# Kernel optimization log

Hardware: AMD Instinct MI355X
Metric: run time of the kernel (lower is better)

The kernel has to match this reference:

```python
import jax, jax.numpy as jnp
import numpy as np

D_MODEL = 1024
NUM_HEADS = 16
D_K = D_MODEL // NUM_HEADS


def setup_inputs() -> dict:
    key = jax.random.key(0)
    ks = jax.random.split(key, 5)
    B, S = 4, 2048
    scale = 1.0 / np.sqrt(D_MODEL)
    x = jax.random.normal(ks[0], (B, S, D_MODEL), dtype=jnp.float32)
    # Linear(d_model, d_model, bias=False) weights, stored as [out, in] like torch
    Wq = jax.random.normal(ks[1], (D_MODEL, D_MODEL), dtype=jnp.float32) * scale
    Wk = jax.random.normal(ks[2], (D_MODEL, D_MODEL), dtype=jnp.float32) * scale
    Wv = jax.random.normal(ks[3], (D_MODEL, D_MODEL), dtype=jnp.float32) * scale
    Wo = jax.random.normal(ks[4], (D_MODEL, D_MODEL), dtype=jnp.float32) * scale
    return {"x": x, "Wq": Wq, "Wk": Wk, "Wv": Wv, "Wo": Wo}


def reference(x, Wq, Wk, Wv, Wo):
    B, S, D = x.shape
    H, dk = NUM_HEADS, D_K
    # projections (torch Linear: x @ W.T)
    q = (x @ Wq.T).reshape(B, S, H, dk).transpose(0, 2, 1, 3)  # [B,H,S,dk]
    k = (x @ Wk.T).reshape(B, S, H, dk).transpose(0, 2, 1, 3)
    v = (x @ Wv.T).reshape(B, S, H, dk).transpose(0, 2, 1, 3)
    scores = jnp.einsum("bhqd,bhkd->bhqk", q, k) / jnp.sqrt(jnp.float32(dk))
    causal = jnp.triu(jnp.ones((S, S), dtype=bool), k=1)  # True above diagonal -> masked
    scores = jnp.where(causal[None, None], -jnp.inf, scores)
    attn = jax.nn.softmax(scores, axis=-1)
    out = jnp.einsum("bhqk,bhkd->bhqd", attn, v)  # [B,H,S,dk]
    out = out.transpose(0, 2, 1, 3).reshape(B, S, D)
    return out @ Wo.T
```

## Files before the change

kernel.cpp:

```cpp
#include <hip/hip_runtime.h>

typedef __bf16 bf16_t;
typedef __bf16 bf16x8 __attribute__((ext_vector_type(8)));
typedef __bf16 bf16x4 __attribute__((ext_vector_type(4)));
typedef float f32x4 __attribute__((ext_vector_type(4)));
typedef unsigned short u16x8 __attribute__((ext_vector_type(8)));

#define AS1C(p) ((const __attribute__((address_space(1))) void*)(p))
#define AS3(p) ((__attribute__((address_space(3))) void*)(p))

__device__ __forceinline__ unsigned short f2b_rne(float f) {
  union { float f; unsigned u; } x; x.f = f;
  unsigned u = x.u;
  u += 0x7fffu + ((u >> 16) & 1u);
  return (unsigned short)(u >> 16);
}

__device__ __forceinline__ float fast_exp2(float x) {
  return __builtin_amdgcn_exp2f(x);
}

__global__ __launch_bounds__(256) void cast_f32_bf16(const float* __restrict__ in,
                                                     unsigned short* __restrict__ out,
                                                     int n) {
  int i = (blockIdx.x * 256 + threadIdx.x) * 8;
  if (i >= n) return;
  const float4* p = reinterpret_cast<const float4*>(in + i);
  float4 a = p[0], b = p[1];
  u16x8 o;
  o[0] = f2b_rne(a.x); o[1] = f2b_rne(a.y); o[2] = f2b_rne(a.z); o[3] = f2b_rne(a.w);
  o[4] = f2b_rne(b.x); o[5] = f2b_rne(b.y); o[6] = f2b_rne(b.z); o[7] = f2b_rne(b.w);
  *reinterpret_cast<u16x8*>(out + i) = o;
}

__global__ __launch_bounds__(256) void cast_w4(const float* __restrict__ w0,
                                               const float* __restrict__ w1,
                                               const float* __restrict__ w2,
                                               const float* __restrict__ w3,
                                               unsigned short* __restrict__ out) {
  const float* in = (blockIdx.y == 0) ? w0 : (blockIdx.y == 1) ? w1
                  : (blockIdx.y == 2) ? w2 : w3;
  int i = (blockIdx.x * 256 + threadIdx.x) * 8;
  unsigned short* o = out + (size_t)blockIdx.y * (1024u * 1024u);
  const float4* p = reinterpret_cast<const float4*>(in + i);
  float4 a = p[0], b = p[1];
  u16x8 v;
  v[0] = f2b_rne(a.x); v[1] = f2b_rne(a.y); v[2] = f2b_rne(a.z); v[3] = f2b_rne(a.w);
  v[4] = f2b_rne(b.x); v[5] = f2b_rne(b.y); v[6] = f2b_rne(b.z); v[7] = f2b_rne(b.w);
  *reinterpret_cast<u16x8*>(o + i) = v;
}

template <int OUT_F32>
__global__ __launch_bounds__(256) void gemm_bt(const bf16_t* __restrict__ A,
                                               const bf16_t* __restrict__ Bm,
                                               void* __restrict__ C,
                                               int M, int N, int K, int lda,
                                               float scale, int qlim) {
  __shared__ bf16_t As[128 * 32];
  __shared__ bf16_t Bs[128 * 32];
  const int tid = threadIdx.x;
  const int lane = tid & 63, wave = tid >> 6;
  const int wm = wave >> 1, wn = wave & 1;
  const int r = lane & 15, kg = lane >> 4;
  const int m0 = blockIdx.y * 128, n0 = blockIdx.x * 128;
  const float sc = (n0 < qlim) ? scale : 1.0f;
  f32x4 acc[4][4] = {};
  const size_t abase = (size_t)m0 * lda;
  const size_t bbase = (size_t)n0 * K;
  for (int k0 = 0; k0 < K; k0 += 32) {
#pragma unroll
    for (int c = 0; c < 2; ++c) {
      int e = (c * 256 + tid) * 8;
      int rr = e >> 5, cc = e & 31;
      __builtin_amdgcn_global_load_lds(AS1C(A + abase + (size_t)rr * lda + k0 + cc),
                                       AS3(As + (c * 256 + wave * 64) * 8), 16, 0, 0);
      __builtin_amdgcn_global_load_lds(AS1C(Bm + bbase + (size_t)rr * K + k0 + cc),
                                       AS3(Bs + (c * 256 + wave * 64) * 8), 16, 0, 0);
    }
    __syncthreads();
    bf16x8 af[4], bfr[4];
#pragma unroll
    for (int t = 0; t < 4; ++t) {
      af[t]  = *reinterpret_cast<const bf16x8*>(As + (wm * 64 + t * 16 + r) * 32 + kg * 8);
      bfr[t] = *reinterpret_cast<const bf16x8*>(Bs + (wn * 64 + t * 16 + r) * 32 + kg * 8);
    }
    __builtin_amdgcn_s_setprio(1);
#pragma unroll
    for (int i = 0; i < 4; ++i)
#pragma unroll
      for (int j = 0; j < 4; ++j)
        acc[i][j] = __builtin_amdgcn_mfma_f32_16x16x32_bf16(af[i], bfr[j], acc[i][j], 0, 0, 0);
    __builtin_amdgcn_s_setprio(0);
    __syncthreads();
  }
#pragma unroll
  for (int i = 0; i < 4; ++i) {
#pragma unroll
    for (int j = 0; j < 4; ++j) {
      const int mb = m0 + wm * 64 + i * 16 + kg * 4;
      const int nc = n0 + wn * 64 + j * 16 + r;
#pragma unroll
      for (int v = 0; v < 4; ++v) {
        float val = acc[i][j][v] * sc;
        size_t idx = (size_t)(mb + v) * N + nc;
        if (OUT_F32) reinterpret_cast<float*>(C)[idx] = val;
        else reinterpret_cast<unsigned short*>(C)[idx] = f2b_rne(val);
      }
    }
  }
}

__global__ __launch_bounds__(256) void transpose_v(const bf16_t* __restrict__ qkv,
                                                   bf16_t* __restrict__ vt) {
  __shared__ bf16_t Vs[64 * 72];
  const int t = threadIdx.x;
  const int s0 = blockIdx.x * 64;
  const int bh = blockIdx.y;
  const int b = bh >> 4, h = bh & 15;
  const size_t in_base = ((size_t)b * 2048 + s0) * 3072 + 2048 + h * 64;
#pragma unroll
  for (int c = 0; c < 2; ++c) {
    int chunk = c * 256 + t;
    int ss = chunk >> 3, dd = (chunk & 7) * 8;
    bf16x8 v = *reinterpret_cast<const bf16x8*>(qkv + in_base + (size_t)ss * 3072 + dd);
    *reinterpret_cast<bf16x8*>(Vs + ss * 72 + dd) = v;
  }
  __syncthreads();
  const size_t out_base = (size_t)bh * 64 * 2048 + s0;
#pragma unroll
  for (int c = 0; c < 2; ++c) {
    int chunk = c * 256 + t;
    int dd = chunk >> 3, ss = (chunk & 7) * 8;
    bf16x8 o;
#pragma unroll
    for (int j = 0; j < 8; ++j) o[j] = Vs[(ss + j) * 72 + dd];
    *reinterpret_cast<bf16x8*>(vt + out_base + (size_t)dd * 2048 + ss) = o;
  }
}

__global__ __launch_bounds__(512) void flash_attn(const bf16_t* __restrict__ QKV,
                                                  const bf16_t* __restrict__ VT,
                                                  unsigned short* __restrict__ O,
                                                  int ostride) {
  __shared__ bf16_t Ks[64 * 72];
  __shared__ bf16_t Vts[64 * 72];
  __shared__ bf16_t Pl[8][16 * 72];
  const int tid = threadIdx.x;
  const int lane = tid & 63, wave = tid >> 6;
  const int r = lane & 15, kg = lane >> 4;
  const int xcd = blockIdx.x & 7;
  const int bh = xcd * 8 + (blockIdx.y & 7);
  const int qt = 15 - ((blockIdx.x >> 3) * 8 + (blockIdx.y >> 3));
  const int b = bh >> 4, h = bh & 15;
  const size_t qkv_row0 = (size_t)b * 2048 * 3072;
  const int qcol = h * 64, kcol = 1024 + h * 64;
  const size_t vt_base = (size_t)bh * 64 * 2048;
  const size_t o_row0 = (size_t)b * 2048 * ostride;
  const int ocol = h * 64;
  const int srr = tid >> 3, scc = (tid & 7) * 8;

  const int q0 = qt * 128;
  const int qrow = q0 + wave * 16 + r;
  const int tmax_w = (q0 + wave * 16 + 15) >> 6;
  const int ntiles = qt * 2 + 2;

  const size_t qoff = qkv_row0 + (size_t)qrow * 3072 + qcol;
  bf16x8 qf0 = *reinterpret_cast<const bf16x8*>(QKV + qoff + kg * 8);
  bf16x8 qf1 = *reinterpret_cast<const bf16x8*>(QKV + qoff + 32 + kg * 8);

  f32x4 oacc[4] = {};
  float m_run = -3e30f, l_run = 0.f;

  bf16x8 gk = *reinterpret_cast<const bf16x8*>(QKV + qkv_row0 + (size_t)srr * 3072 + kcol + scc);
  bf16x8 gv = *reinterpret_cast<const bf16x8*>(VT + vt_base + (size_t)srr * 2048 + scc);

  for (int t = 0; t < ntiles; ++t) {
    __syncthreads();
    *reinterpret_cast<bf16x8*>(Ks + srr * 72 + scc) = gk;
    *reinterpret_cast<bf16x8*>(Vts + srr * 72 + scc) = gv;
    __syncthreads();
    if (t + 1 < ntiles) {
      const int kv1 = (t + 1) * 64;
      gk = *reinterpret_cast<const bf16x8*>(QKV + qkv_row0 + (size_t)(kv1 + srr) * 3072 + kcol + scc);
      gv = *reinterpret_cast<const bf16x8*>(VT + vt_base + (size_t)srr * 2048 + kv1 + scc);
    }
    if (t > tmax_w) continue;

    const int kv0 = t * 64;
    float vals[16];
#pragma unroll
    for (int nt = 0; nt < 4; ++nt) {
      bf16x8 kf0 = *reinterpret_cast<const bf16x8*>(Ks + (nt * 16 + r) * 72 + kg * 8);
      bf16x8 kf1 = *reinterpret_cast<const bf16x8*>(Ks + (nt * 16 + r) * 72 + 32 + kg * 8);
      f32x4 s = {};
      __builtin_amdgcn_s_setprio(1);
      s = __builtin_amdgcn_mfma_f32_16x16x32_bf16(kf0, qf0, s, 0, 0, 0);
      s = __builtin_amdgcn_mfma_f32_16x16x32_bf16(kf1, qf1, s, 0, 0, 0);
      __builtin_amdgcn_s_setprio(0);
#pragma unroll
      for (int v = 0; v < 4; ++v) vals[nt * 4 + v] = s[v];
    }
    if (t == tmax_w) {
#pragma unroll
      for (int nt = 0; nt < 4; ++nt)
#pragma unroll
        for (int v = 0; v < 4; ++v)
          if (kv0 + nt * 16 + kg * 4 + v > qrow) vals[nt * 4 + v] = -3e30f;
    }
    float a0 = fmaxf(fmaxf(vals[0], vals[1]), vals[2]);
    float a1 = fmaxf(fmaxf(vals[3], vals[4]), vals[5]);
    float a2 = fmaxf(fmaxf(vals[6], vals[7]), vals[8]);
    float a3 = fmaxf(fmaxf(vals[9], vals[10]), vals[11]);
    float a4 = fmaxf(fmaxf(vals[12], vals[13]), vals[14]);
    float pmax = fmaxf(fmaxf(fmaxf(a0, a1), fmaxf(a2, a3)), fmaxf(a4, vals[15]));
    pmax = fmaxf(pmax, __shfl_xor(pmax, 16));
    pmax = fmaxf(pmax, __shfl_xor(pmax, 32));
    if (!__all(pmax <= m_run + 8.0f)) {
      const float m_new = fmaxf(m_run, pmax);
      const float alpha = fast_exp2(m_run - m_new);
      l_run *= alpha;
      f32x4 al;
#pragma unroll
      for (int v = 0; v < 4; ++v) al[v] = __shfl(alpha, kg * 4 + v);
#pragma unroll
      for (int dt = 0; dt < 4; ++dt)
#pragma unroll
        for (int v = 0; v < 4; ++v) oacc[dt][v] *= al[v];
      m_run = m_new;
    }
    float psum = 0.f;
#pragma unroll
    for (int ii = 0; ii < 16; ++ii) {
      float p = fast_exp2(vals[ii] - m_run);
      vals[ii] = p;
      psum += p;
    }
    psum += __shfl_xor(psum, 16);
    psum += __shfl_xor(psum, 32);
    l_run += psum;

#pragma unroll
    for (int nt = 0; nt < 4; ++nt) {
      bf16x4 pb;
#pragma unroll
      for (int v = 0; v < 4; ++v) pb[v] = (bf16_t)vals[nt * 4 + v];
      *reinterpret_cast<bf16x4*>(&Pl[wave][r * 72 + nt * 16 + kg * 4]) = pb;
    }
    bf16x8 pa0 = *reinterpret_cast<const bf16x8*>(&Pl[wave][r * 72 + kg * 8]);
    bf16x8 pa1 = *reinterpret_cast<const bf16x8*>(&Pl[wave][r * 72 + 32 + kg * 8]);

#pragma unroll
    for (int dt = 0; dt < 4; ++dt) {
      bf16x8 vb0 = *reinterpret_cast<const bf16x8*>(Vts + (dt * 16 + r) * 72 + kg * 8);
      bf16x8 vb1 = *reinterpret_cast<const bf16x8*>(Vts + (dt * 16 + r) * 72 + 32 + kg * 8);
      __builtin_amdgcn_s_setprio(1);
      oacc[dt] = __builtin_amdgcn_mfma_f32_16x16x32_bf16(pa0, vb0, oacc[dt], 0, 0, 0);
      oacc[dt] = __builtin_amdgcn_mfma_f32_16x16x32_bf16(pa1, vb1, oacc[dt], 0, 0, 0);
      __builtin_amdgcn_s_setprio(0);
    }
  }

  const float linv = 1.0f / l_run;
  f32x4 il;
#pragma unroll
  for (int v = 0; v < 4; ++v) il[v] = __shfl(linv, kg * 4 + v);
  const size_t orow0 = o_row0 + (size_t)(q0 + wave * 16) * ostride + ocol;
#pragma unroll
  for (int dt = 0; dt < 4; ++dt) {
    const int d = dt * 16 + r;
#pragma unroll
    for (int v = 0; v < 4; ++v)
      O[orow0 + (size_t)(kg * 4 + v) * ostride + d] = f2b_rne(oacc[dt][v] * il[v]);
  }
}

extern "C" void kernel_launch(void* const* d_in, const int* in_sizes, int n_in,
                              void* d_out, int out_size, void* d_ws, size_t ws_size,
                              hipStream_t stream) {
  const float* x  = (const float*)d_in[0];
  const float* Wq = (const float*)d_in[1];
  const float* Wk = (const float*)d_in[2];
  const float* Wv = (const float*)d_in[3];
  const float* Wo = (const float*)d_in[4];

  char* ws = (char*)d_ws;
  bf16_t* xb  = (bf16_t*)(ws);
  bf16_t* wqb = (bf16_t*)(ws + (16u << 20));
  bf16_t* wob = (bf16_t*)(ws + (22u << 20));
  bf16_t* qkv = (bf16_t*)(ws + (24u << 20));
  bf16_t* vt  = (bf16_t*)(ws);

  const int NX = 4 * 2048 * 1024;
  cast_f32_bf16<<<NX / 2048, 256, 0, stream>>>(x, (unsigned short*)xb, NX);
  cast_w4<<<dim3(512, 4), 256, 0, stream>>>(Wq, Wk, Wv, Wo, (unsigned short*)wqb);

  gemm_bt<0><<<dim3(3072 / 128, 8192 / 128), 256, 0, stream>>>(
      xb, wqb, qkv, 8192, 3072, 1024, 1024, 0.18033688011112042f, 1024);

  transpose_v<<<dim3(2048 / 64, 64), 256, 0, stream>>>(qkv, vt);

  flash_attn<<<dim3(16, 64), 512, 0, stream>>>(qkv, vt, (unsigned short*)qkv, 3072);

  gemm_bt<1><<<dim3(1024 / 128, 8192 / 128), 256, 0, stream>>>(
      qkv, wob, d_out, 8192, 1024, 1024, 3072, 1.0f, 0);
}
```

Baseline: 213.9 us.

## Pair causal query tiles per block and double-buffer K/V tiles in LDS

Each flash-attention block now handles two query tiles, qt and 15-qt, one after the other. This balances the causal workload across blocks, with a 64x8 grid instead of 16x64, and drops the previous XCD-aware block remapping. K and V shared-memory tiles are double-buffered so each iteration needs one barrier instead of two. The row-sum reduction is deferred to the end as a per-lane partial sum, and the max shuffles run only when a rescale is needed. The risks are fewer blocks in flight, lost L2 locality from the old XCD mapping, and more LDS use per block.

```diff
diff --git a/kernel.cpp b/kernel.cpp
--- a/kernel.cpp
+++ b/kernel.cpp
@@ -142,15 +142,14 @@
                                                   const bf16_t* __restrict__ VT,
                                                   unsigned short* __restrict__ O,
                                                   int ostride) {
-  __shared__ bf16_t Ks[64 * 72];
-  __shared__ bf16_t Vts[64 * 72];
+  __shared__ bf16_t Ks[2][64 * 72];
+  __shared__ bf16_t Vts[2][64 * 72];
   __shared__ bf16_t Pl[8][16 * 72];
   const int tid = threadIdx.x;
   const int lane = tid & 63, wave = tid >> 6;
   const int r = lane & 15, kg = lane >> 4;
-  const int xcd = blockIdx.x & 7;
-  const int bh = xcd * 8 + (blockIdx.y & 7);
-  const int qt = 15 - ((blockIdx.x >> 3) * 8 + (blockIdx.y >> 3));
+  const int bh = blockIdx.x;
+  const int pair = blockIdx.y;
   const int b = bh >> 4, h = bh & 15;
   const size_t qkv_row0 = (size_t)b * 2048 * 3072;
   const int qcol = h * 64, kcol = 1024 + h * 64;
@@ -159,118 +158,120 @@
   const int ocol = h * 64;
   const int srr = tid >> 3, scc = (tid & 7) * 8;
 
-  const int q0 = qt * 128;
-  const int qrow = q0 + wave * 16 + r;
-  const int tmax_w = (q0 + wave * 16 + 15) >> 6;
-  const int ntiles = qt * 2 + 2;
-
-  const size_t qoff = qkv_row0 + (size_t)qrow * 3072 + qcol;
-  bf16x8 qf0 = *reinterpret_cast<const bf16x8*>(QKV + qoff + kg * 8);
-  bf16x8 qf1 = *reinterpret_cast<const bf16x8*>(QKV + qoff + 32 + kg * 8);
-
-  f32x4 oacc[4] = {};
-  float m_run = -3e30f, l_run = 0.f;
-
-  bf16x8 gk = *reinterpret_cast<const bf16x8*>(QKV + qkv_row0 + (size_t)srr * 3072 + kcol + scc);
-  bf16x8 gv = *reinterpret_cast<const bf16x8*>(VT + vt_base + (size_t)srr * 2048 + scc);
-
-  for (int t = 0; t < ntiles; ++t) {
-    __syncthreads();
-    *reinterpret_cast<bf16x8*>(Ks + srr * 72 + scc) = gk;
-    *reinterpret_cast<bf16x8*>(Vts + srr * 72 + scc) = gv;
-    __syncthreads();
-    if (t + 1 < ntiles) {
-      const int kv1 = (t + 1) * 64;
-      gk = *reinterpret_cast<const bf16x8*>(QKV + qkv_row0 + (size_t)(kv1 + srr) * 3072 + kcol + scc);
-      gv = *reinterpret_cast<const bf16x8*>(VT + vt_base + (size_t)srr * 2048 + kv1 + scc);
-    }
-    if (t > tmax_w) continue;
-
-    const int kv0 = t * 64;
-    float vals[16];
-#pragma unroll
-    for (int nt = 0; nt < 4; ++nt) {
-      bf16x8 kf0 = *reinterpret_cast<const bf16x8*>(Ks + (nt * 16 + r) * 72 + kg * 8);
-      bf16x8 kf1 = *reinterpret_cast<const bf16x8*>(Ks + (nt * 16 + r) * 72 + 32 + kg * 8);
-      f32x4 s = {};
-      __builtin_amdgcn_s_setprio(1);
-      s = __builtin_amdgcn_mfma_f32_16x16x32_bf16(kf0, qf0, s, 0, 0, 0);
-      s = __builtin_amdgcn_mfma_f32_16x16x32_bf16(kf1, qf1, s, 0, 0, 0);
-      __builtin_amdgcn_s_setprio(0);
-#pragma unroll
-      for (int v = 0; v < 4; ++v) vals[nt * 4 + v] = s[v];
-    }
-    if (t == tmax_w) {
-#pragma unroll
-      for (int nt = 0; nt < 4; ++nt)
-#pragma unroll
-        for (int v = 0; v < 4; ++v)
-          if (kv0 + nt * 16 + kg * 4 + v > qrow) vals[nt * 4 + v] = -3e30f;
-    }
-    float a0 = fmaxf(fmaxf(vals[0], vals[1]), vals[2]);
-    float a1 = fmaxf(fmaxf(vals[3], vals[4]), vals[5]);
-    float a2 = fmaxf(fmaxf(vals[6], vals[7]), vals[8]);
-    float a3 = fmaxf(fmaxf(vals[9], vals[10]), vals[11]);
-    float a4 = fmaxf(fmaxf(vals[12], vals[13]), vals[14]);
-    float pmax = fmaxf(fmaxf(fmaxf(a0, a1), fmaxf(a2, a3)), fmaxf(a4, vals[15]));
-    pmax = fmaxf(pmax, __shfl_xor(pmax, 16));
-    pmax = fmaxf(pmax, __shfl_xor(pmax, 32));
-    if (!__all(pmax <= m_run + 8.0f)) {
-      const float m_new = fmaxf(m_run, pmax);
-      const float alpha = fast_exp2(m_run - m_new);
-      l_run *= alpha;
-      f32x4 al;
-#pragma unroll
-      for (int v = 0; v < 4; ++v) al[v] = __shfl(alpha, kg * 4 + v);
-#pragma unroll
-      for (int dt = 0; dt < 4; ++dt)
-#pragma unroll
-        for (int v = 0; v < 4; ++v) oacc[dt][v] *= al[v];
-      m_run = m_new;
-    }
-    float psum = 0.f;
-#pragma unroll
-    for (int ii = 0; ii < 16; ++ii) {
-      float p = fast_exp2(vals[ii] - m_run);
-      vals[ii] = p;
-      psum += p;
-    }
-    psum += __shfl_xor(psum, 16);
-    psum += __shfl_xor(psum, 32);
-    l_run += psum;
-
-#pragma unroll
-    for (int nt = 0; nt < 4; ++nt) {
-      bf16x4 pb;
-#pragma unroll
-      for (int v = 0; v < 4; ++v) pb[v] = (bf16_t)vals[nt * 4 + v];
-      *reinterpret_cast<bf16x4*>(&Pl[wave][r * 72 + nt * 16 + kg * 4]) = pb;
-    }
-    bf16x8 pa0 = *reinterpret_cast<const bf16x8*>(&Pl[wave][r * 72 + kg * 8]);
-    bf16x8 pa1 = *reinterpret_cast<const bf16x8*>(&Pl[wave][r * 72 + 32 + kg * 8]);
-
+  for (int pass = 0; pass < 2; ++pass) {
+    const int qt = pass ? (15 - pair) : pair;
+    const int q0 = qt * 128;
+    const int qrow = q0 + wave * 16 + r;
+    const int tmax_w = (q0 + wave * 16 + 15) >> 6;
+    const int ntiles = qt * 2 + 2;
+
+    const size_t qoff = qkv_row0 + (size_t)qrow * 3072 + qcol;
+    bf16x8 qf0 = *reinterpret_cast<const bf16x8*>(QKV + qoff + kg * 8);
+    bf16x8 qf1 = *reinterpret_cast<const bf16x8*>(QKV + qoff + 32 + kg * 8);
+
+    f32x4 oacc[4] = {};
+    float m_run = -3e30f, l_lane = 0.f;
+
+    bf16x8 gk = *reinterpret_cast<const bf16x8*>(QKV + qkv_row0 + (size_t)srr * 3072 + kcol + scc);
+    bf16x8 gv = *reinterpret_cast<const bf16x8*>(VT + vt_base + (size_t)srr * 2048 + scc);
+
+    for (int t = 0; t < ntiles; ++t) {
+      const int buf = t & 1;
+      *reinterpret_cast<bf16x8*>(&Ks[buf][srr * 72 + scc]) = gk;
+      *reinterpret_cast<bf16x8*>(&Vts[buf][srr * 72 + scc]) = gv;
+      __syncthreads();
+      if (t + 1 < ntiles) {
+        const int kv1 = (t + 1) * 64;
+        gk = *reinterpret_cast<const bf16x8*>(QKV + qkv_row0 + (size_t)(kv1 + srr) * 3072 + kcol + scc);
+        gv = *reinterpret_cast<const bf16x8*>(VT + vt_base + (size_t)srr * 2048 + kv1 + scc);
+      }
+      if (t > tmax_w) continue;
+
+      const int kv0 = t * 64;
+      float vals[16];
+#pragma unroll
+      for (int nt = 0; nt < 4; ++nt) {
+        bf16x8 kf0 = *reinterpret_cast<const bf16x8*>(&Ks[buf][(nt * 16 + r) * 72 + kg * 8]);
+        bf16x8 kf1 = *reinterpret_cast<const bf16x8*>(&Ks[buf][(nt * 16 + r) * 72 + 32 + kg * 8]);
+        f32x4 s = {};
+        __builtin_amdgcn_s_setprio(1);
+        s = __builtin_amdgcn_mfma_f32_16x16x32_bf16(kf0, qf0, s, 0, 0, 0);
+        s = __builtin_amdgcn_mfma_f32_16x16x32_bf16(kf1, qf1, s, 0, 0, 0);
+        __builtin_amdgcn_s_setprio(0);
+#pragma unroll
+        for (int v = 0; v < 4; ++v) vals[nt * 4 + v] = s[v];
+      }
+      if (t == tmax_w) {
+#pragma unroll
+        for (int nt = 0; nt < 4; ++nt)
+#pragma unroll
+          for (int v = 0; v < 4; ++v)
+            if (kv0 + nt * 16 + kg * 4 + v > qrow) vals[nt * 4 + v] = -3e30f;
+      }
+      float a0 = fmaxf(fmaxf(vals[0], vals[1]), vals[2]);
+      float a1 = fmaxf(fmaxf(vals[3], vals[4]), vals[5]);
+      float a2 = fmaxf(fmaxf(vals[6], vals[7]), vals[8]);
+      float a3 = fmaxf(fmaxf(vals[9], vals[10]), vals[11]);
+      float a4 = fmaxf(fmaxf(vals[12], vals[13]), vals[14]);
+      float pmax = fmaxf(fmaxf(fmaxf(a0, a1), fmaxf(a2, a3)), fmaxf(a4, vals[15]));
+      if (!__all(pmax <= m_run + 8.0f)) {
+        pmax = fmaxf(pmax, __shfl_xor(pmax, 16));
+        pmax = fmaxf(pmax, __shfl_xor(pmax, 32));
+        const float m_new = fmaxf(m_run, pmax);
+        const float alpha = fast_exp2(m_run - m_new);
+        l_lane *= alpha;
+        f32x4 al;
+#pragma unroll
+        for (int v = 0; v < 4; ++v) al[v] = __shfl(alpha, kg * 4 + v);
+#pragma unroll
+        for (int dt = 0; dt < 4; ++dt)
+#pragma unroll
+          for (int v = 0; v < 4; ++v) oacc[dt][v] *= al[v];
+        m_run = m_new;
+      }
+#pragma unroll
+      for (int ii = 0; ii < 16; ++ii) {
+        float p = fast_exp2(vals[ii] - m_run);
+        vals[ii] = p;
+        l_lane += p;
+      }
+
+#pragma unroll
+      for (int nt = 0; nt < 4; ++nt) {
+        bf16x4 pb;
+#pragma unroll
+        for (int v = 0; v < 4; ++v) pb[v] = (bf16_t)vals[nt * 4 + v];
+        *reinterpret_cast<bf16x4*>(&Pl[wave][r * 72 + nt * 16 + kg * 4]) = pb;
+      }
+      bf16x8 pa0 = *reinterpret_cast<const bf16x8*>(&Pl[wave][r * 72 + kg * 8]);
+      bf16x8 pa1 = *reinterpret_cast<const bf16x8*>(&Pl[wave][r * 72 + 32 + kg * 8]);
+
+#pragma unroll
+      for (int dt = 0; dt < 4; ++dt) {
+        bf16x8 vb0 = *reinterpret_cast<const bf16x8*>(&Vts[buf][(dt * 16 + r) * 72 + kg * 8]);
+        bf16x8 vb1 = *reinterpret_cast<const bf16x8*>(&Vts[buf][(dt * 16 + r) * 72 + 32 + kg * 8]);
+        __builtin_amdgcn_s_setprio(1);
+        oacc[dt] = __builtin_amdgcn_mfma_f32_16x16x32_bf16(pa0, vb0, oacc[dt], 0, 0, 0);
+        oacc[dt] = __builtin_amdgcn_mfma_f32_16x16x32_bf16(pa1, vb1, oacc[dt], 0, 0, 0);
+        __builtin_amdgcn_s_setprio(0);
+      }
+    }
+
+    float l_row = l_lane;
+    l_row += __shfl_xor(l_row, 16);
+    l_row += __shfl_xor(l_row, 32);
+    const float linv = 1.0f / l_row;
+    f32x4 il;
+#pragma unroll
+    for (int v = 0; v < 4; ++v) il[v] = __shfl(linv, kg * 4 + v);
+    const size_t orow0 = o_row0 + (size_t)(q0 + wave * 16) * ostride + ocol;
 #pragma unroll
     for (int dt = 0; dt < 4; ++dt) {
-      bf16x8 vb0 = *reinterpret_cast<const bf16x8*>(Vts + (dt * 16 + r) * 72 + kg * 8);
-      bf16x8 vb1 = *reinterpret_cast<const bf16x8*>(Vts + (dt * 16 + r) * 72 + 32 + kg * 8);
-      __builtin_amdgcn_s_setprio(1);
-      oacc[dt] = __builtin_amdgcn_mfma_f32_16x16x32_bf16(pa0, vb0, oacc[dt], 0, 0, 0);
-      oacc[dt] = __builtin_amdgcn_mfma_f32_16x16x32_bf16(pa1, vb1, oacc[dt], 0, 0, 0);
-      __builtin_amdgcn_s_setprio(0);
-    }
-  }
-
-  const float linv = 1.0f / l_run;
-  f32x4 il;
-#pragma unroll
-  for (int v = 0; v < 4; ++v) il[v] = __shfl(linv, kg * 4 + v);
-  const size_t orow0 = o_row0 + (size_t)(q0 + wave * 16) * ostride + ocol;
-#pragma unroll
-  for (int dt = 0; dt < 4; ++dt) {
-    const int d = dt * 16 + r;
-#pragma unroll
-    for (int v = 0; v < 4; ++v)
-      O[orow0 + (size_t)(kg * 4 + v) * ostride + d] = f2b_rne(oacc[dt][v] * il[v]);
+      const int d = dt * 16 + r;
+#pragma unroll
+      for (int v = 0; v < 4; ++v)
+        O[orow0 + (size_t)(kg * 4 + v) * ostride + d] = f2b_rne(oacc[dt][v] * il[v]);
+    }
   }
 }
 
@@ -299,7 +300,7 @@
 
   transpose_v<<<dim3(2048 / 64, 64), 256, 0, stream>>>(qkv, vt);
 
-  flash_attn<<<dim3(16, 64), 512, 0, stream>>>(qkv, vt, (unsigned short*)qkv, 3072);
+  flash_attn<<<dim3(64, 8), 512, 0, stream>>>(qkv, vt, (unsigned short*)qkv, 3072);
 
   gemm_bt<1><<<dim3(1024 / 128, 8192 / 128), 256, 0, stream>>>(
       qkv, wob, d_out, 8192, 1024, 1024, 3072, 1.0f, 0);
```

After: 186.8 us. 1.15x faster.
